# Kernel tuning notes

Measured on AMD Instinct MI355X. Metric: run time of the kernel, lower is better.

The kernel has to match this reference:

```python
import jax, jax.numpy as jnp
import numpy as np

KK = 9   # kH * kW
P = 2    # num_points (len(dilations))


def setup_inputs() -> dict:
    key = jax.random.key(0)
    ks = jax.random.split(key, 12)
    N, A, C, OC = 8000, 4000, 256, 256
    R, rH, rW = 64, 64, 64
    inp = {}
    inp["in_core_feats"] = jax.random.normal(ks[0], (N, C), jnp.float32)
    inp["aux_feats"] = jax.random.normal(ks[1], (A, C), jnp.float32)
    # offset MLP: near-zero weights, bias plays role of the dilation-grid init offsets
    inp["off_w"] = 0.01 * jax.random.normal(ks[2], (KK * P * 2, C), jnp.float32)
    inp["off_b"] = 2.0 * jax.random.uniform(ks[3], (KK * P * 2,), jnp.float32) - 1.0
    inp["pw_w"] = 0.01 * jax.random.normal(ks[4], (KK * P, C), jnp.float32)
    inp["pw_b"] = jnp.zeros((KK * P,), jnp.float32)
    inp["mw_w"] = 0.01 * jax.random.normal(ks[5], (KK, C), jnp.float32)
    inp["mw_b"] = jnp.zeros((KK,), jnp.float32)
    inp["weight"] = jax.random.normal(ks[6], (OC, KK * C), jnp.float32) / np.sqrt(KK * C)
    inp["bias"] = 0.01 * jax.random.normal(ks[7], (OC,), jnp.float32)
    inp["id_map"] = jax.random.randint(ks[8], (R, rH, rW), 0, N + A)
    inp["roi_ids"] = jax.random.randint(ks[9], (N,), 0, R)
    inp["pos_ids"] = jax.random.randint(ks[10], (N, 2), 0, rW)
    return inp


def reference(in_core_feats, aux_feats, off_w, off_b, pw_w, pw_b, mw_w, mw_b,
              weight, bias, id_map, roi_ids, pos_ids):
    N, C = in_core_feats.shape
    # predicted sampling locations in RoI (x, y) coords: [N, KK, P, 2]
    conv_xy = (in_core_feats @ off_w.T + off_b).reshape(N, KK, P, 2)
    conv_xy = pos_ids.astype(conv_xy.dtype)[:, None, None, :] + conv_xy
    floor_xy = jnp.floor(conv_xy)
    base_ids = floor_xy.astype(jnp.int32)
    grid = jnp.array([[0, 0], [1, 0], [0, 1], [1, 1]], jnp.int32)
    cids = base_ids[:, :, :, None, :] + grid            # [N, KK, P, 4, 2]
    cx, cy = cids[..., 0], cids[..., 1]
    rH, rW = id_map.shape[1], id_map.shape[2]
    pad = (cx < 0) | (cy < 0) | (cx >= rW) | (cy >= rH)
    cx = jnp.clip(cx, 0, rW - 1)
    cy = jnp.clip(cy, 0, rH - 1)
    gids = id_map[roi_ids[:, None, None, None], cy, cx]  # [N, KK, P, 4]
    pad_idx = N + aux_feats.shape[0]
    gids = jnp.where(pad, pad_idx, gids)
    # interpolation weights, literal translation of the torch indexing
    delta = conv_xy - floor_xy                           # [N, KK, P, 2]
    dstk = jnp.stack([delta, 1.0 - delta], axis=3)       # [N, KK, P, 2, 2]
    x_ids = jnp.array([1, 0, 1, 0])
    y_ids = jnp.array([1, 1, 0, 0])
    w = dstk[:, :, :, 0, :][..., x_ids] * dstk[:, :, :, 1, :][..., y_ids]  # [N, KK, P, 4]
    # point weights (softmax over points) and modulation weights (sigmoid)
    pw = jax.nn.softmax((in_core_feats @ pw_w.T + pw_b).reshape(N, KK, P), axis=2)
    w = pw[..., None] * w
    mw = jax.nn.sigmoid(in_core_feats @ mw_w.T + mw_b)   # [N, KK]
    w = mw[:, :, None, None] * w
    # gather + weighted reduce over points and corners, then dense matmul
    all_feats = jnp.concatenate(
        [in_core_feats, aux_feats, jnp.zeros((1, C), in_core_feats.dtype)], axis=0)
    sampled = jnp.einsum('nkpgc,nkpg->nkc', all_feats[gids], w)  # [N, KK, C]
    out = sampled.reshape(N, KK * C) @ weight.T + bias
    return out
```

## Files before the change

kernel.cpp:

```cpp
#include <hip/hip_runtime.h>

typedef __attribute__((ext_vector_type(8))) short short8;
typedef __attribute__((ext_vector_type(4))) float f32x4;

static __device__ __forceinline__ unsigned short f2b(float f) {
  union { float f; unsigned int u; } v; v.f = f;
  unsigned int u = v.u;
  unsigned int r = (u + 0x7FFFu + ((u >> 16) & 1u)) >> 16;
  return (unsigned short)r;
}
static __device__ __forceinline__ float b2f(unsigned short u) {
  union { unsigned int u; float f; } v; v.u = ((unsigned int)u) << 16;
  return v.f;
}

__global__ __launch_bounds__(256) void prep_kernel(
    const float* __restrict__ core, const float* __restrict__ aux,
    const float* __restrict__ wgt,
    unsigned short* __restrict__ tab, unsigned short* __restrict__ wB)
{
  const long TAB = 12001L * 256;
  const long WN  = 256L * 2304;
  long i = ((long)blockIdx.x * 256 + threadIdx.x) * 4;
  float4 v;
  unsigned short* dst;
  if (i < TAB) {
    long row = i >> 8;
    if (row < 8000)        v = *(const float4*)(core + i);
    else if (row < 12000)  v = *(const float4*)(aux + (i - 8000L * 256));
    else                   v = make_float4(0.f, 0.f, 0.f, 0.f);
    dst = tab + i;
  } else {
    long j = i - TAB;
    if (j >= WN) return;
    v = *(const float4*)(wgt + j);
    dst = wB + j;
  }
  ushort4 o = make_ushort4(f2b(v.x), f2b(v.y), f2b(v.z), f2b(v.w));
  *(ushort4*)dst = o;
}

__global__ __launch_bounds__(256) void proj_kernel(
    const float* __restrict__ core,
    const float* __restrict__ off_w, const float* __restrict__ off_b,
    const float* __restrict__ pw_w,  const float* __restrict__ pw_b,
    const float* __restrict__ mw_w,  const float* __restrict__ mw_b,
    const int* __restrict__ id_map, const int* __restrict__ roi_ids,
    const int* __restrict__ pos_ids,
    int* __restrict__ gids, float* __restrict__ wts)
{
  __shared__ float dots[32][64];
  const int tid  = threadIdx.x;
  const int lane = tid & 63;
  const int wv   = tid >> 6;
  const int nbase = blockIdx.x * 32 + wv * 8;

  float acc[8] = {0.f,0.f,0.f,0.f,0.f,0.f,0.f,0.f};
  if (lane < 63) {
    const float* wr; float bb;
    if (lane < 36)      { wr = off_w + lane * 256;       bb = off_b[lane]; }
    else if (lane < 54) { wr = pw_w + (lane - 36) * 256; bb = pw_b[lane - 36]; }
    else                { wr = mw_w + (lane - 54) * 256; bb = mw_b[lane - 54]; }
    const float4* w4 = (const float4*)wr;
    #pragma unroll 4
    for (int i = 0; i < 64; ++i) {
      const float4 w = w4[i];
      #pragma unroll
      for (int r = 0; r < 8; ++r) {
        const float4 x = *(const float4*)(core + (long)(nbase + r) * 256 + i * 4);
        acc[r] += w.x * x.x + w.y * x.y + w.z * x.z + w.w * x.w;
      }
    }
    #pragma unroll
    for (int r = 0; r < 8; ++r) acc[r] += bb;
  }
  #pragma unroll
  for (int r = 0; r < 8; ++r) dots[wv * 8 + r][lane] = acc[r];
  __syncthreads();

  #pragma unroll
  for (int round = 0; round < 3; ++round) {
    int task = round * 256 + tid;
    if (task < 576) {
      int nl = task / 18;
      int kp = task - nl * 18;
      int k = kp >> 1, p = kp & 1;
      int n = blockIdx.x * 32 + nl;
      float x = dots[nl][k*4 + p*2 + 0] + (float)pos_ids[n*2 + 0];
      float y = dots[nl][k*4 + p*2 + 1] + (float)pos_ids[n*2 + 1];
      float fx = floorf(x), fy = floorf(y);
      float dx = x - fx, dy = y - fy;
      int bx = (int)fx, by = (int)fy;
      float l0 = dots[nl][36 + k*2], l1 = dots[nl][36 + k*2 + 1];
      float mmax = fmaxf(l0, l1);
      float e0 = __expf(l0 - mmax), e1 = __expf(l1 - mmax);
      float pwv = (p ? e1 : e0) / (e0 + e1);
      float mwv = 1.f / (1.f + __expf(-dots[nl][54 + k]));
      float wb  = pwv * mwv;
      const int* imap = id_map + roi_ids[n] * 4096;
      int base = ((n * 9 + k) * 2 + p) * 4;
      #pragma unroll
      for (int g = 0; g < 4; ++g) {
        int gx = g & 1, gy = g >> 1;
        int cx = bx + gx, cy = by + gy;
        bool pad = ((cx | cy) < 0) | (cx >= 64) | (cy >= 64);
        int cxc = min(max(cx, 0), 63), cyc = min(max(cy, 0), 63);
        int gid = pad ? 12000 : imap[cyc * 64 + cxc];
        float f1 = gx ? dx : dy;
        float f2 = gy ? (1.f - dx) : (1.f - dy);
        gids[base + g] = gid;
        wts[base + g]  = wb * f1 * f2;
      }
    }
  }
}

__global__ __launch_bounds__(256) void gather_kernel(
    const unsigned short* __restrict__ tab,
    const int* __restrict__ gids, const float* __restrict__ wts,
    unsigned short* __restrict__ sampled)
{
  const int lane = threadIdx.x & 63;
  const int wv   = threadIdx.x >> 6;
  const int n    = blockIdx.x * 4 + wv;
  const int c    = lane * 4;
  #pragma unroll
  for (int k = 0; k < 9; ++k) {
    const int jb = (n * 9 + k) * 8;
    float a0 = 0.f, a1 = 0.f, a2 = 0.f, a3 = 0.f;
    #pragma unroll
    for (int j = 0; j < 8; ++j) {
      const int gid = gids[jb + j];
      const float w = wts[jb + j];
      const ushort4 t = *(const ushort4*)(tab + (long)gid * 256 + c);
      a0 += w * b2f(t.x); a1 += w * b2f(t.y);
      a2 += w * b2f(t.z); a3 += w * b2f(t.w);
    }
    ushort4 o = make_ushort4(f2b(a0), f2b(a1), f2b(a2), f2b(a3));
    *(ushort4*)(sampled + ((long)n * 2304 + k * 256 + c)) = o;
  }
}

__global__ __launch_bounds__(256) void gemm_kernel(
    const unsigned short* __restrict__ S,
    const unsigned short* __restrict__ W,
    const float* __restrict__ bias,
    float* __restrict__ out)
{
  __shared__ __align__(16) unsigned short As[64][72];
  __shared__ __align__(16) unsigned short Bs[64][72];
  const int m0 = blockIdx.x * 64;
  const int n0 = blockIdx.y * 64;
  const int t    = threadIdx.x;
  const int lane = t & 63;
  const int wv   = t >> 6;
  const int wr   = wv >> 1, wc = wv & 1;

  f32x4 acc[2][2] = {};

  const int srow = t >> 3;
  const int schk = t & 7;

  for (int kt = 0; kt < 36; ++kt) {
    const int k0 = kt * 64;
    const uint4 ra0 = *(const uint4*)(S + (long)(m0 + srow)      * 2304 + k0 + schk * 8);
    const uint4 ra1 = *(const uint4*)(S + (long)(m0 + srow + 32) * 2304 + k0 + schk * 8);
    const uint4 rb0 = *(const uint4*)(W + (long)(n0 + srow)      * 2304 + k0 + schk * 8);
    const uint4 rb1 = *(const uint4*)(W + (long)(n0 + srow + 32) * 2304 + k0 + schk * 8);
    __syncthreads();
    *(uint4*)&As[srow][schk * 8]      = ra0;
    *(uint4*)&As[srow + 32][schk * 8] = ra1;
    *(uint4*)&Bs[srow][schk * 8]      = rb0;
    *(uint4*)&Bs[srow + 32][schk * 8] = rb1;
    __syncthreads();
    #pragma unroll
    for (int kc = 0; kc < 2; ++kc) {
      const int kk = kc * 32 + (lane >> 4) * 8;
      short8 af[2], bf[2];
      af[0] = *(const short8*)&As[wr * 32 + (lane & 15)][kk];
      af[1] = *(const short8*)&As[wr * 32 + 16 + (lane & 15)][kk];
      bf[0] = *(const short8*)&Bs[wc * 32 + (lane & 15)][kk];
      bf[1] = *(const short8*)&Bs[wc * 32 + 16 + (lane & 15)][kk];
      #pragma unroll
      for (int i = 0; i < 2; ++i)
        #pragma unroll
        for (int j = 0; j < 2; ++j)
          acc[i][j] = __builtin_amdgcn_mfma_f32_16x16x32_bf16(af[i], bf[j], acc[i][j], 0, 0, 0);
    }
  }

  #pragma unroll
  for (int i = 0; i < 2; ++i) {
    const int row = m0 + wr * 32 + i * 16 + (lane >> 4) * 4;
    #pragma unroll
    for (int j = 0; j < 2; ++j) {
      const int col = n0 + wc * 32 + j * 16 + (lane & 15);
      const float bs = bias[col];
      #pragma unroll
      for (int r = 0; r < 4; ++r) {
        out[(long)(row + r) * 256 + col] = acc[i][j][r] + bs;
      }
    }
  }
}

extern "C" void kernel_launch(void* const* d_in, const int* in_sizes, int n_in,
                              void* d_out, int out_size, void* d_ws, size_t ws_size,
                              hipStream_t stream)
{
  const float* core   = (const float*)d_in[0];
  const float* aux    = (const float*)d_in[1];
  const float* off_w  = (const float*)d_in[2];
  const float* off_b  = (const float*)d_in[3];
  const float* pw_w   = (const float*)d_in[4];
  const float* pw_b   = (const float*)d_in[5];
  const float* mw_w   = (const float*)d_in[6];
  const float* mw_b   = (const float*)d_in[7];
  const float* wgt    = (const float*)d_in[8];
  const float* bias   = (const float*)d_in[9];
  const int* id_map   = (const int*)d_in[10];
  const int* roi_ids  = (const int*)d_in[11];
  const int* pos_ids  = (const int*)d_in[12];
  char* ws = (char*)d_ws;

  unsigned short* tab     = (unsigned short*)(ws);
  unsigned short* wB      = (unsigned short*)(ws + 6144512);
  int*            gids    = (int*)           (ws + 7324160);
  float*          wts     = (float*)         (ws + 9628160);
  unsigned short* sampled = (unsigned short*)(ws + 11932160);
  float* out = (float*)d_out;

  hipLaunchKernelGGL(prep_kernel, dim3(3577), dim3(256), 0, stream,
                     core, aux, wgt, tab, wB);
  hipLaunchKernelGGL(proj_kernel, dim3(250), dim3(256), 0, stream,
                     core, off_w, off_b, pw_w, pw_b, mw_w, mw_b,
                     id_map, roi_ids, pos_ids, gids, wts);
  hipLaunchKernelGGL(gather_kernel, dim3(2000), dim3(256), 0, stream,
                     tab, gids, wts, sampled);
  hipLaunchKernelGGL(gemm_kernel, dim3(125, 4), dim3(256), 0, stream,
                     sampled, wB, bias, out);
}
```

Before: 176.0 us.

## Fuse bilinear gather into the GEMM, producing A tiles on the fly

Merges the gather and GEMM kernels. Each 512-thread block builds its 32-row A tile in shared memory directly from the bf16 feature table using the gids/weights, and holds the full 256-column B slab. This removes the sampled intermediate's global write and re-read and one launch, and register-prefetches the next tile's gathers and weights. In exchange the grid drops to 250 blocks, so fewer are resident across the CUs, and each block reloads all of W.

```diff
diff --git a/kernel.cpp b/kernel.cpp
--- a/kernel.cpp
+++ b/kernel.cpp
@@ -115,92 +115,98 @@
   }
 }
 
-__global__ __launch_bounds__(256) void gather_kernel(
+__global__ __launch_bounds__(512) void gg_kernel(
     const unsigned short* __restrict__ tab,
+    const unsigned short* __restrict__ W,
     const int* __restrict__ gids, const float* __restrict__ wts,
-    unsigned short* __restrict__ sampled)
-{
-  const int lane = threadIdx.x & 63;
-  const int wv   = threadIdx.x >> 6;
-  const int n    = blockIdx.x * 4 + wv;
-  const int c    = lane * 4;
-  #pragma unroll
-  for (int k = 0; k < 9; ++k) {
-    const int jb = (n * 9 + k) * 8;
-    float a0 = 0.f, a1 = 0.f, a2 = 0.f, a3 = 0.f;
-    #pragma unroll
-    for (int j = 0; j < 8; ++j) {
-      const int gid = gids[jb + j];
-      const float w = wts[jb + j];
-      const ushort4 t = *(const ushort4*)(tab + (long)gid * 256 + c);
-      a0 += w * b2f(t.x); a1 += w * b2f(t.y);
-      a2 += w * b2f(t.z); a3 += w * b2f(t.w);
-    }
-    ushort4 o = make_ushort4(f2b(a0), f2b(a1), f2b(a2), f2b(a3));
-    *(ushort4*)(sampled + ((long)n * 2304 + k * 256 + c)) = o;
-  }
-}
-
-__global__ __launch_bounds__(256) void gemm_kernel(
-    const unsigned short* __restrict__ S,
-    const unsigned short* __restrict__ W,
-    const float* __restrict__ bias,
-    float* __restrict__ out)
-{
-  __shared__ __align__(16) unsigned short As[64][72];
-  __shared__ __align__(16) unsigned short Bs[64][72];
-  const int m0 = blockIdx.x * 64;
-  const int n0 = blockIdx.y * 64;
+    const float* __restrict__ bias, float* __restrict__ out)
+{
+  __shared__ __align__(16) unsigned short As[32][72];
+  __shared__ __align__(16) unsigned short Bs[256][72];
+
   const int t    = threadIdx.x;
+  const int m0   = blockIdx.x * 32;
+  const int row  = t >> 4;
+  const int q    = t & 15;
+  const int bn   = t >> 1;
+  const int bh   = t & 1;
   const int lane = t & 63;
   const int wv   = t >> 6;
-  const int wr   = wv >> 1, wc = wv & 1;
-
-  f32x4 acc[2][2] = {};
-
-  const int srow = t >> 3;
-  const int schk = t & 7;
+  const int wr   = wv >> 2;
+  const int wc   = wv & 3;
+
+  f32x4 acc[4] = {};
+
+  const long grow = (long)(m0 + row) * 72;
+  int   gid[8]; float w[8];
+  ushort4 tv[8];
+  uint4   bv[4];
+
+  #pragma unroll
+  for (int j = 0; j < 8; ++j) { gid[j] = gids[grow + j]; w[j] = wts[grow + j]; }
+  {
+    const int c = q * 4;
+    #pragma unroll
+    for (int j = 0; j < 8; ++j)
+      tv[j] = *(const ushort4*)(tab + (long)gid[j] * 256 + c);
+    #pragma unroll
+    for (int u = 0; u < 4; ++u)
+      bv[u] = *(const uint4*)(W + (long)bn * 2304 + bh * 32 + u * 8);
+  }
 
   for (int kt = 0; kt < 36; ++kt) {
-    const int k0 = kt * 64;
-    const uint4 ra0 = *(const uint4*)(S + (long)(m0 + srow)      * 2304 + k0 + schk * 8);
-    const uint4 ra1 = *(const uint4*)(S + (long)(m0 + srow + 32) * 2304 + k0 + schk * 8);
-    const uint4 rb0 = *(const uint4*)(W + (long)(n0 + srow)      * 2304 + k0 + schk * 8);
-    const uint4 rb1 = *(const uint4*)(W + (long)(n0 + srow + 32) * 2304 + k0 + schk * 8);
     __syncthreads();
-    *(uint4*)&As[srow][schk * 8]      = ra0;
-    *(uint4*)&As[srow + 32][schk * 8] = ra1;
-    *(uint4*)&Bs[srow][schk * 8]      = rb0;
-    *(uint4*)&Bs[srow + 32][schk * 8] = rb1;
+    {
+      float a0 = 0.f, a1 = 0.f, a2 = 0.f, a3 = 0.f;
+      #pragma unroll
+      for (int j = 0; j < 8; ++j) {
+        a0 += w[j] * b2f(tv[j].x); a1 += w[j] * b2f(tv[j].y);
+        a2 += w[j] * b2f(tv[j].z); a3 += w[j] * b2f(tv[j].w);
+      }
+      *(ushort4*)&As[row][q * 4] = make_ushort4(f2b(a0), f2b(a1), f2b(a2), f2b(a3));
+      #pragma unroll
+      for (int u = 0; u < 4; ++u)
+        *(uint4*)&Bs[bn][bh * 32 + u * 8] = bv[u];
+    }
     __syncthreads();
+    const int nkt = kt + 1;
+    if (nkt < 36) {
+      if ((nkt & 3) == 0) {
+        const int tap = nkt >> 2;
+        #pragma unroll
+        for (int j = 0; j < 8; ++j) {
+          gid[j] = gids[grow + tap * 8 + j];
+          w[j] = wts[grow + tap * 8 + j];
+        }
+      }
+      const int c = (nkt & 3) * 64 + q * 4;
+      #pragma unroll
+      for (int j = 0; j < 8; ++j)
+        tv[j] = *(const ushort4*)(tab + (long)gid[j] * 256 + c);
+      #pragma unroll
+      for (int u = 0; u < 4; ++u)
+        bv[u] = *(const uint4*)(W + (long)bn * 2304 + nkt * 64 + bh * 32 + u * 8);
+    }
     #pragma unroll
     for (int kc = 0; kc < 2; ++kc) {
       const int kk = kc * 32 + (lane >> 4) * 8;
-      short8 af[2], bf[2];
-      af[0] = *(const short8*)&As[wr * 32 + (lane & 15)][kk];
-      af[1] = *(const short8*)&As[wr * 32 + 16 + (lane & 15)][kk];
-      bf[0] = *(const short8*)&Bs[wc * 32 + (lane & 15)][kk];
-      bf[1] = *(const short8*)&Bs[wc * 32 + 16 + (lane & 15)][kk];
-      #pragma unroll
-      for (int i = 0; i < 2; ++i)
-        #pragma unroll
-        for (int j = 0; j < 2; ++j)
-          acc[i][j] = __builtin_amdgcn_mfma_f32_16x16x32_bf16(af[i], bf[j], acc[i][j], 0, 0, 0);
-    }
-  }
-
-  #pragma unroll
-  for (int i = 0; i < 2; ++i) {
-    const int row = m0 + wr * 32 + i * 16 + (lane >> 4) * 4;
-    #pragma unroll
-    for (int j = 0; j < 2; ++j) {
-      const int col = n0 + wc * 32 + j * 16 + (lane & 15);
-      const float bs = bias[col];
-      #pragma unroll
-      for (int r = 0; r < 4; ++r) {
-        out[(long)(row + r) * 256 + col] = acc[i][j][r] + bs;
-      }
-    }
+      const short8 af = *(const short8*)&As[wr * 16 + (lane & 15)][kk];
+      #pragma unroll
+      for (int nf = 0; nf < 4; ++nf) {
+        const short8 bf = *(const short8*)&Bs[wc * 64 + nf * 16 + (lane & 15)][kk];
+        acc[nf] = __builtin_amdgcn_mfma_f32_16x16x32_bf16(af, bf, acc[nf], 0, 0, 0);
+      }
+    }
+  }
+
+  const int orow = m0 + wr * 16 + (lane >> 4) * 4;
+  #pragma unroll
+  for (int nf = 0; nf < 4; ++nf) {
+    const int col = wc * 64 + nf * 16 + (lane & 15);
+    const float bs = bias[col];
+    #pragma unroll
+    for (int r = 0; r < 4; ++r)
+      out[(long)(orow + r) * 256 + col] = acc[nf][r] + bs;
   }
 }
 
@@ -223,20 +229,17 @@
   const int* pos_ids  = (const int*)d_in[12];
   char* ws = (char*)d_ws;
 
-  unsigned short* tab     = (unsigned short*)(ws);
-  unsigned short* wB      = (unsigned short*)(ws + 6144512);
-  int*            gids    = (int*)           (ws + 7324160);
-  float*          wts     = (float*)         (ws + 9628160);
-  unsigned short* sampled = (unsigned short*)(ws + 11932160);
+  unsigned short* tab = (unsigned short*)(ws);
+  unsigned short* wB  = (unsigned short*)(ws + 6144512);
+  int*            gd  = (int*)           (ws + 7324160);
+  float*          wt  = (float*)         (ws + 9628160);
   float* out = (float*)d_out;
 
   hipLaunchKernelGGL(prep_kernel, dim3(3577), dim3(256), 0, stream,
                      core, aux, wgt, tab, wB);
   hipLaunchKernelGGL(proj_kernel, dim3(250), dim3(256), 0, stream,
                      core, off_w, off_b, pw_w, pw_b, mw_w, mw_b,
-                     id_map, roi_ids, pos_ids, gids, wts);
-  hipLaunchKernelGGL(gather_kernel, dim3(2000), dim3(256), 0, stream,
-                     tab, gids, wts, sampled);
-  hipLaunchKernelGGL(gemm_kernel, dim3(125, 4), dim3(256), 0, stream,
-                     sampled, wB, bias, out);
-}
+                     id_map, roi_ids, pos_ids, gd, wt);
+  hipLaunchKernelGGL(gg_kernel, dim3(250), dim3(512), 0, stream,
+                     tab, wB, gd, wt, bias, out);
+}
```

Measured after the change: 251.8 us. 1.43x slower.
